# Kernel optimization log

Measured on AMD Instinct MI355X. Metric: run time of the kernel, lower is better.

Reference implementation:

```python
import jax, jax.numpy as jnp
import numpy as np

B_, S, D_IN, D_OUT, R = 4, 2048, 2048, 2048, 16

def setup_inputs() -> dict:
    key = jax.random.key(0)
    k = jax.random.split(key, 5)
    x = jax.random.normal(k[0], (B_, S, D_IN), dtype=jnp.float32)
    W = jax.random.normal(k[1], (D_OUT, D_IN), dtype=jnp.float32) * (1.0 / np.sqrt(D_IN))
    b = jax.random.normal(k[2], (D_OUT,), dtype=jnp.float32) * 0.02
    A = jax.random.normal(k[3], (R, D_IN), dtype=jnp.float32) * 0.02  # nn.init.normal_(std=0.02)
    Bm = jax.random.normal(k[4], (D_OUT, R), dtype=jnp.float32) * 0.02
    scale = jnp.asarray(0.8, dtype=jnp.float32)
    return {"x": x, "W": W, "b": b, "A": A, "B": Bm, "scale": scale}

def reference(x, W, b, A, B, scale):
    # base linear: y = x @ W^T + b
    orig = jnp.einsum('bsd,od->bso', x, W) + b
    # LoRA: scale * (x @ A^T) @ B^T
    h = jnp.einsum('bsd,rd->bsr', x, A)          # [B,S,r]
    lora = jnp.einsum('bsr,or->bso', h, B) * scale
    return orig + lora
```

## Files before the change

kernel.cpp:

```cpp
#include <hip/hip_runtime.h>
#include <hip/hip_bf16.h>
#include <cstdint>


typedef __bf16 bf16x8 __attribute__((ext_vector_type(8)));
typedef float floatx4 __attribute__((ext_vector_type(4)));
typedef unsigned short ushort8 __attribute__((ext_vector_type(8)));

#define BM 256
#define BN 256
#define BK 64
#define NT 32

__device__ __forceinline__ void gload_lds16(const void* g, void* l) {
    __builtin_amdgcn_global_load_lds((__attribute__((address_space(1))) void*)g,
                                     (__attribute__((address_space(3))) void*)l,
                                     16, 0, 0);
}

__device__ __forceinline__ unsigned short f2bf_bits(float f) {
    unsigned int u = __float_as_uint(f);
    u += 0x7FFFu + ((u >> 16) & 1u);
    return (unsigned short)(u >> 16);
}

__global__ __launch_bounds__(256)
void aux_kernel(const float* __restrict__ x, unsigned short* __restrict__ Xbf,
                const float* __restrict__ W, const float* __restrict__ A,
                const float* __restrict__ Bm, const float* __restrict__ scale_p,
                unsigned short* __restrict__ Weff)
{
    const int K = 2048, R = 16;
    int bid = blockIdx.x;
    if (bid < 8192) {
        size_t i = ((size_t)bid * 256 + threadIdx.x) * 8;
        float4 a = *reinterpret_cast<const float4*>(x + i);
        float4 b = *reinterpret_cast<const float4*>(x + i + 4);
        ushort8 o;
        o[0] = f2bf_bits(a.x); o[1] = f2bf_bits(a.y);
        o[2] = f2bf_bits(a.z); o[3] = f2bf_bits(a.w);
        o[4] = f2bf_bits(b.x); o[5] = f2bf_bits(b.y);
        o[6] = f2bf_bits(b.z); o[7] = f2bf_bits(b.w);
        *reinterpret_cast<ushort8*>(Xbf + i) = o;
    } else {
        int t  = (bid - 8192) * 256 + threadIdx.x;
        int n  = t >> 8;
        int k8 = (t & 255) << 3;

        float s = *scale_p;
        float br[16];
#pragma unroll
        for (int r = 0; r < R; ++r)
            br[r] = s * Bm[n * R + r];

        float acc[8] = {0,0,0,0,0,0,0,0};
#pragma unroll
        for (int r = 0; r < R; ++r) {
            const float* ap = A + r * K + k8;
#pragma unroll
            for (int j = 0; j < 8; ++j)
                acc[j] += br[r] * ap[j];
        }

        const float* wp = W + (size_t)n * K + k8;
        ushort8 o;
#pragma unroll
        for (int j = 0; j < 8; ++j)
            o[j] = f2bf_bits(wp[j] + acc[j]);
        *reinterpret_cast<ushort8*>(Weff + (size_t)n * K + k8) = o;
    }
}

#define BAR()       __builtin_amdgcn_s_barrier()
#define WAIT_LGKM() asm volatile("s_waitcnt lgkmcnt(0)" ::: "memory")
#define WAIT_VM4()  asm volatile("s_waitcnt vmcnt(4)" ::: "memory")
#define WAIT_VM0()  asm volatile("s_waitcnt vmcnt(0)" ::: "memory")

#define STAGE_A(buf, mh, kt) do {                                             \
    gload_lds16(gA0 + (size_t)(mh) * 64 * K + (kt) * 64, &Sa[buf][mh][c0 * 8]); \
    gload_lds16(gA1 + (size_t)(mh) * 64 * K + (kt) * 64, &Sa[buf][mh][c1 * 8]); \
} while (0)

#define STAGE_B(buf, nh, kt) do {                                             \
    gload_lds16(gB0 + (size_t)(nh) * 32 * K + (kt) * 64, &Sb[buf][nh][c0 * 8]); \
    gload_lds16(gB1 + (size_t)(nh) * 32 * K + (kt) * 64, &Sb[buf][nh][c1 * 8]); \
} while (0)

#define READ_A(buf, mh) do {                                                  \
    const unsigned short* ra = &Sa[buf][mh][(wr * 64 + lrow) * 64];           \
    _Pragma("unroll")                                                         \
    for (int mq = 0; mq < 4; ++mq) {                                          \
        af[0][mq] = *reinterpret_cast<const bf16x8*>(ra + mq * 1024 + swz0);  \
        af[1][mq] = *reinterpret_cast<const bf16x8*>(ra + mq * 1024 + swz1);  \
    }                                                                         \
} while (0)

#define READ_B(buf, nh) do {                                                  \
    const unsigned short* rb = &Sb[buf][nh][(wc * 32 + lrow) * 64];           \
    _Pragma("unroll")                                                         \
    for (int nq = 0; nq < 2; ++nq) {                                          \
        bq[0][nq] = *reinterpret_cast<const bf16x8*>(rb + nq * 1024 + swz0);  \
        bq[1][nq] = *reinterpret_cast<const bf16x8*>(rb + nq * 1024 + swz1);  \
    }                                                                         \
} while (0)

#define MFMAQ(mh, nh) do {                                                    \
    __builtin_amdgcn_s_setprio(1);                                            \
    _Pragma("unroll")                                                         \
    for (int mq = 0; mq < 4; ++mq)                                            \
        _Pragma("unroll")                                                     \
        for (int nq = 0; nq < 2; ++nq) {                                      \
            floatx4 tmp = __builtin_amdgcn_mfma_f32_16x16x32_bf16(            \
                af[0][mq], bq[0][nq], acc[(mh)*4+mq][(nh)*2+nq], 0, 0, 0);    \
            acc[(mh)*4+mq][(nh)*2+nq] = __builtin_amdgcn_mfma_f32_16x16x32_bf16( \
                af[1][mq], bq[1][nq], tmp, 0, 0, 0);                          \
        }                                                                     \
    __builtin_amdgcn_s_setprio(0);                                            \
} while (0)

__global__ __launch_bounds__(512)
void gemm_bias_kernel(const unsigned short* __restrict__ X,
                      const unsigned short* __restrict__ Wt,
                      const float* __restrict__ bias,
                      float* __restrict__ out)
{
    const int N = 2048, K = 2048;

    __shared__ alignas(16) unsigned short Sa[2][2][8192];
    __shared__ alignas(16) unsigned short Sb[2][2][8192];

    const int tid  = threadIdx.x;
    const int wave = tid >> 6;
    const int lane = tid & 63;
    const int lrow = lane & 15;
    const int quad = lane >> 4;
    const int wr   = wave >> 2;
    const int wc   = wave & 3;

    const int id  = blockIdx.x;
    const int xcd = id & 7;
    const int sg  = id >> 3;
    const int bm  = (xcd * 4 + (sg & 3)) * BM;
    const int bn  = (sg >> 2) * BN;

    const int c0 = tid, c1 = tid + 512;
    const int ar0 = (c0 >> 3) & 63, as0 = c0 & 7;
    const int ar1 = (c1 >> 3) & 63, as1 = c1 & 7;
    const unsigned short* gA0 = X + (size_t)(bm + (c0 >> 9) * 128 + ar0) * K
                                  + ((as0 ^ (ar0 & 7)) << 3);
    const unsigned short* gA1 = X + (size_t)(bm + (c1 >> 9) * 128 + ar1) * K
                                  + ((as1 ^ (ar1 & 7)) << 3);
    const int br0 = (c0 >> 3) & 31, br1 = (c1 >> 3) & 31;
    const unsigned short* gB0 = Wt + (size_t)(bn + (c0 >> 8) * 64 + br0) * K
                                   + ((as0 ^ (br0 & 7)) << 3);
    const unsigned short* gB1 = Wt + (size_t)(bn + (c1 >> 8) * 64 + br1) * K
                                   + ((as1 ^ (br1 & 7)) << 3);

    const int swz0 = (quad ^ (lrow & 7)) << 3;
    const int swz1 = swz0 ^ 32;

    floatx4 acc[8][4] = {};
    bf16x8 af[2][4];
    bf16x8 bq[2][2];

    STAGE_A(0, 0, 0);
    STAGE_B(0, 1, 0);
    STAGE_B(0, 0, 0);
    STAGE_A(0, 1, 0);
    STAGE_A(1, 0, 1);
    STAGE_B(1, 1, 1);
    WAIT_VM4(); BAR();

#pragma unroll 1
    for (int tt = 0; tt < NT; tt += 2) {
        const int t1 = tt + 1;
        const int t2 = (tt + 2 < NT) ? tt + 2 : NT - 1;
        const int t3 = (tt + 3 < NT) ? tt + 3 : NT - 1;

        READ_A(0, 0); READ_B(0, 0);
        STAGE_B(1, 0, t1);
        BAR(); WAIT_LGKM(); MFMAQ(0, 0); BAR();
        READ_B(0, 1);
        STAGE_A(1, 1, t1);
        BAR(); WAIT_LGKM(); MFMAQ(0, 1); BAR();
        READ_A(0, 1);
        STAGE_A(0, 0, t2);
        BAR(); WAIT_LGKM(); MFMAQ(1, 1); BAR();
        READ_B(0, 0);
        STAGE_B(0, 1, t2);
        BAR(); WAIT_LGKM(); MFMAQ(1, 0); WAIT_VM4(); BAR();

        READ_A(1, 0); READ_B(1, 0);
        STAGE_B(0, 0, t2);
        BAR(); WAIT_LGKM(); MFMAQ(0, 0); BAR();
        READ_B(1, 1);
        STAGE_A(0, 1, t2);
        BAR(); WAIT_LGKM(); MFMAQ(0, 1); BAR();
        READ_A(1, 1);
        STAGE_A(1, 0, t3);
        BAR(); WAIT_LGKM(); MFMAQ(1, 1); BAR();
        READ_B(1, 0);
        STAGE_B(1, 1, t3);
        BAR(); WAIT_LGKM(); MFMAQ(1, 0); WAIT_VM4(); BAR();
    }
    WAIT_VM0();

    float bsv[4];
#pragma unroll
    for (int ni = 0; ni < 4; ++ni)
        bsv[ni] = bias[bn + wc * 64 + (ni >> 1) * 32 + (ni & 1) * 16 + lrow];

    const int rbase = quad << 2;
#pragma unroll
    for (int mi = 0; mi < 8; ++mi) {
#pragma unroll
        for (int r = 0; r < 4; ++r) {
            size_t rowoff = (size_t)(bm + wr * 128 + (mi >> 2) * 64
                                     + (mi & 3) * 16 + rbase + r) * N;
#pragma unroll
            for (int ni = 0; ni < 4; ++ni)
                out[rowoff + bn + wc * 64 + (ni >> 1) * 32 + (ni & 1) * 16 + lrow]
                    = acc[mi][ni][r] + bsv[ni];
        }
    }
}

extern "C" void kernel_launch(void* const* d_in, const int* in_sizes, int n_in,
                              void* d_out, int out_size, void* d_ws, size_t ws_size,
                              hipStream_t stream)
{
    const float* x  = (const float*)d_in[0];
    const float* W  = (const float*)d_in[1];
    const float* b  = (const float*)d_in[2];
    const float* A  = (const float*)d_in[3];
    const float* Bm = (const float*)d_in[4];
    const float* sc = (const float*)d_in[5];
    float* out = (float*)d_out;

    const size_t M = 8192, N = 2048, K = 2048;

    unsigned short* Xbf  = (unsigned short*)d_ws;
    unsigned short* Weff = (unsigned short*)d_ws + M * K;

    aux_kernel<<<dim3((M * K + N * K) / 8 / 256), dim3(256), 0, stream>>>(
        x, Xbf, W, A, Bm, sc, Weff);

    gemm_bias_kernel<<<dim3((M / BM) * (N / BN)), dim3(512), 0, stream>>>(
        Xbf, Weff, b, out);
}
```

Measured before the change: 207.5 us.

## Fuse x fp32-to-bf16 conversion into GEMM A-tile loading via registers

Removes the separate pass that converted x to bf16 in a workspace. The GEMM now loads fp32 x tiles into registers, converts them to bf16 and writes them to swizzled LDS, interleaved with the MFMA phases. It also sets launch_bounds to allow two blocks per CU. The aim is to skip the write and re-read of a 32MB bf16 copy of x, at the cost of reading fp32 x (twice the bytes) several times across N-tiles, plus more register pressure and VALU work inside the main loop. The vmcnt waits were also dropped, so correctness now relies on the register-data dependencies and barriers.

```diff
diff --git a/kernel.cpp b/kernel.cpp
--- a/kernel.cpp
+++ b/kernel.cpp
@@ -25,65 +25,65 @@
 }
 
 __global__ __launch_bounds__(256)
-void aux_kernel(const float* __restrict__ x, unsigned short* __restrict__ Xbf,
-                const float* __restrict__ W, const float* __restrict__ A,
+void aux_kernel(const float* __restrict__ W, const float* __restrict__ A,
                 const float* __restrict__ Bm, const float* __restrict__ scale_p,
                 unsigned short* __restrict__ Weff)
 {
     const int K = 2048, R = 16;
-    int bid = blockIdx.x;
-    if (bid < 8192) {
-        size_t i = ((size_t)bid * 256 + threadIdx.x) * 8;
-        float4 a = *reinterpret_cast<const float4*>(x + i);
-        float4 b = *reinterpret_cast<const float4*>(x + i + 4);
-        ushort8 o;
-        o[0] = f2bf_bits(a.x); o[1] = f2bf_bits(a.y);
-        o[2] = f2bf_bits(a.z); o[3] = f2bf_bits(a.w);
-        o[4] = f2bf_bits(b.x); o[5] = f2bf_bits(b.y);
-        o[6] = f2bf_bits(b.z); o[7] = f2bf_bits(b.w);
-        *reinterpret_cast<ushort8*>(Xbf + i) = o;
-    } else {
-        int t  = (bid - 8192) * 256 + threadIdx.x;
-        int n  = t >> 8;
-        int k8 = (t & 255) << 3;
-
-        float s = *scale_p;
-        float br[16];
-#pragma unroll
-        for (int r = 0; r < R; ++r)
-            br[r] = s * Bm[n * R + r];
-
-        float acc[8] = {0,0,0,0,0,0,0,0};
-#pragma unroll
-        for (int r = 0; r < R; ++r) {
-            const float* ap = A + r * K + k8;
-#pragma unroll
-            for (int j = 0; j < 8; ++j)
-                acc[j] += br[r] * ap[j];
-        }
-
-        const float* wp = W + (size_t)n * K + k8;
-        ushort8 o;
+    int t  = blockIdx.x * 256 + threadIdx.x;
+    int n  = t >> 8;
+    int k8 = (t & 255) << 3;
+
+    float s = *scale_p;
+    float br[16];
+#pragma unroll
+    for (int r = 0; r < R; ++r)
+        br[r] = s * Bm[n * R + r];
+
+    float acc[8] = {0,0,0,0,0,0,0,0};
+#pragma unroll
+    for (int r = 0; r < R; ++r) {
+        const float* ap = A + r * K + k8;
 #pragma unroll
         for (int j = 0; j < 8; ++j)
-            o[j] = f2bf_bits(wp[j] + acc[j]);
-        *reinterpret_cast<ushort8*>(Weff + (size_t)n * K + k8) = o;
+            acc[j] += br[r] * ap[j];
     }
+
+    const float* wp = W + (size_t)n * K + k8;
+    ushort8 o;
+#pragma unroll
+    for (int j = 0; j < 8; ++j)
+        o[j] = f2bf_bits(wp[j] + acc[j]);
+    *reinterpret_cast<ushort8*>(Weff + (size_t)n * K + k8) = o;
 }
 
 #define BAR()       __builtin_amdgcn_s_barrier()
 #define WAIT_LGKM() asm volatile("s_waitcnt lgkmcnt(0)" ::: "memory")
-#define WAIT_VM4()  asm volatile("s_waitcnt vmcnt(4)" ::: "memory")
 #define WAIT_VM0()  asm volatile("s_waitcnt vmcnt(0)" ::: "memory")
 
-#define STAGE_A(buf, mh, kt) do {                                             \
-    gload_lds16(gA0 + (size_t)(mh) * 64 * K + (kt) * 64, &Sa[buf][mh][c0 * 8]); \
-    gload_lds16(gA1 + (size_t)(mh) * 64 * K + (kt) * 64, &Sa[buf][mh][c1 * 8]); \
-} while (0)
-
 #define STAGE_B(buf, nh, kt) do {                                             \
-    gload_lds16(gB0 + (size_t)(nh) * 32 * K + (kt) * 64, &Sb[buf][nh][c0 * 8]); \
-    gload_lds16(gB1 + (size_t)(nh) * 32 * K + (kt) * 64, &Sb[buf][nh][c1 * 8]); \
+    gload_lds16(gB0 + (size_t)(nh) * 32 * 2048 + (kt) * 64, &Sb[buf][nh][c0 * 8]); \
+    gload_lds16(gB1 + (size_t)(nh) * 32 * 2048 + (kt) * 64, &Sb[buf][nh][c1 * 8]); \
+} while (0)
+
+#define AISSUE(mh, kt) do {                                                   \
+    const float* xp = xA + (size_t)(mh) * 64 * 2048 + (kt) * 64;              \
+    q0 = *reinterpret_cast<const float4*>(xp);                                \
+    q1 = *reinterpret_cast<const float4*>(xp + 4);                            \
+    q2 = *reinterpret_cast<const float4*>(xp + 128 * 2048);                   \
+    q3 = *reinterpret_cast<const float4*>(xp + 128 * 2048 + 4);               \
+} while (0)
+
+#define AWRITE(buf, mh) do {                                                  \
+    ushort8 o0, o1;                                                           \
+    o0[0]=f2bf_bits(q0.x); o0[1]=f2bf_bits(q0.y); o0[2]=f2bf_bits(q0.z);      \
+    o0[3]=f2bf_bits(q0.w); o0[4]=f2bf_bits(q1.x); o0[5]=f2bf_bits(q1.y);      \
+    o0[6]=f2bf_bits(q1.z); o0[7]=f2bf_bits(q1.w);                             \
+    o1[0]=f2bf_bits(q2.x); o1[1]=f2bf_bits(q2.y); o1[2]=f2bf_bits(q2.z);      \
+    o1[3]=f2bf_bits(q2.w); o1[4]=f2bf_bits(q3.x); o1[5]=f2bf_bits(q3.y);      \
+    o1[6]=f2bf_bits(q3.z); o1[7]=f2bf_bits(q3.w);                             \
+    *reinterpret_cast<ushort8*>(&Sa[buf][mh][dstA])        = o0;              \
+    *reinterpret_cast<ushort8*>(&Sa[buf][mh][dstA + 4096]) = o1;              \
 } while (0)
 
 #define READ_A(buf, mh) do {                                                  \
@@ -118,8 +118,8 @@
     __builtin_amdgcn_s_setprio(0);                                            \
 } while (0)
 
-__global__ __launch_bounds__(512)
-void gemm_bias_kernel(const unsigned short* __restrict__ X,
+__global__ __launch_bounds__(512, 2)
+void gemm_bias_kernel(const float* __restrict__ x,
                       const unsigned short* __restrict__ Wt,
                       const float* __restrict__ bias,
                       float* __restrict__ out)
@@ -143,18 +143,18 @@
     const int bm  = (xcd * 4 + (sg & 3)) * BM;
     const int bn  = (sg >> 2) * BN;
 
+    const int ar = (tid >> 3) & 63;
+    const int as = tid & 7;
+    const float* xA = x + (size_t)(bm + ar) * K + as * 8;
+    const int dstA = ar * 64 + ((as ^ (ar & 7)) << 3);
+    float4 q0, q1, q2, q3;
+
     const int c0 = tid, c1 = tid + 512;
-    const int ar0 = (c0 >> 3) & 63, as0 = c0 & 7;
-    const int ar1 = (c1 >> 3) & 63, as1 = c1 & 7;
-    const unsigned short* gA0 = X + (size_t)(bm + (c0 >> 9) * 128 + ar0) * K
-                                  + ((as0 ^ (ar0 & 7)) << 3);
-    const unsigned short* gA1 = X + (size_t)(bm + (c1 >> 9) * 128 + ar1) * K
-                                  + ((as1 ^ (ar1 & 7)) << 3);
     const int br0 = (c0 >> 3) & 31, br1 = (c1 >> 3) & 31;
     const unsigned short* gB0 = Wt + (size_t)(bn + (c0 >> 8) * 64 + br0) * K
-                                   + ((as0 ^ (br0 & 7)) << 3);
+                                   + ((as ^ (br0 & 7)) << 3);
     const unsigned short* gB1 = Wt + (size_t)(bn + (c1 >> 8) * 64 + br1) * K
-                                   + ((as1 ^ (br1 & 7)) << 3);
+                                   + (((c1 & 7) ^ (br1 & 7)) << 3);
 
     const int swz0 = (quad ^ (lrow & 7)) << 3;
     const int swz1 = swz0 ^ 32;
@@ -163,13 +163,13 @@
     bf16x8 af[2][4];
     bf16x8 bq[2][2];
 
-    STAGE_A(0, 0, 0);
+    STAGE_B(0, 0, 0);
     STAGE_B(0, 1, 0);
-    STAGE_B(0, 0, 0);
-    STAGE_A(0, 1, 0);
-    STAGE_A(1, 0, 1);
     STAGE_B(1, 1, 1);
-    WAIT_VM4(); BAR();
+    AISSUE(0, 0); AWRITE(0, 0);
+    AISSUE(1, 0); AWRITE(0, 1);
+    AISSUE(0, 1); AWRITE(1, 0);
+    WAIT_VM0(); WAIT_LGKM(); BAR();
 
 #pragma unroll 1
     for (int tt = 0; tt < NT; tt += 2) {
@@ -179,29 +179,33 @@
 
         READ_A(0, 0); READ_B(0, 0);
         STAGE_B(1, 0, t1);
+        AISSUE(1, t1);
         BAR(); WAIT_LGKM(); MFMAQ(0, 0); BAR();
+        AWRITE(1, 1);
         READ_B(0, 1);
-        STAGE_A(1, 1, t1);
+        AISSUE(0, t2);
         BAR(); WAIT_LGKM(); MFMAQ(0, 1); BAR();
+        AWRITE(0, 0);
         READ_A(0, 1);
-        STAGE_A(0, 0, t2);
         BAR(); WAIT_LGKM(); MFMAQ(1, 1); BAR();
         READ_B(0, 0);
         STAGE_B(0, 1, t2);
-        BAR(); WAIT_LGKM(); MFMAQ(1, 0); WAIT_VM4(); BAR();
+        BAR(); WAIT_LGKM(); MFMAQ(1, 0); BAR();
 
         READ_A(1, 0); READ_B(1, 0);
         STAGE_B(0, 0, t2);
+        AISSUE(1, t2);
         BAR(); WAIT_LGKM(); MFMAQ(0, 0); BAR();
+        AWRITE(0, 1);
         READ_B(1, 1);
-        STAGE_A(0, 1, t2);
+        AISSUE(0, t3);
         BAR(); WAIT_LGKM(); MFMAQ(0, 1); BAR();
+        AWRITE(1, 0);
         READ_A(1, 1);
-        STAGE_A(1, 0, t3);
         BAR(); WAIT_LGKM(); MFMAQ(1, 1); BAR();
         READ_B(1, 0);
         STAGE_B(1, 1, t3);
-        BAR(); WAIT_LGKM(); MFMAQ(1, 0); WAIT_VM4(); BAR();
+        BAR(); WAIT_LGKM(); MFMAQ(1, 0); BAR();
     }
     WAIT_VM0();
 
@@ -239,12 +243,11 @@
 
     const size_t M = 8192, N = 2048, K = 2048;
 
-    unsigned short* Xbf  = (unsigned short*)d_ws;
-    unsigned short* Weff = (unsigned short*)d_ws + M * K;
-
-    aux_kernel<<<dim3((M * K + N * K) / 8 / 256), dim3(256), 0, stream>>>(
-        x, Xbf, W, A, Bm, sc, Weff);
+    unsigned short* Weff = (unsigned short*)d_ws;
+
+    aux_kernel<<<dim3(N * K / 8 / 256), dim3(256), 0, stream>>>(
+        W, A, Bm, sc, Weff);
 
     gemm_bias_kernel<<<dim3((M / BM) * (N / BN)), dim3(512), 0, stream>>>(
-        Xbf, Weff, b, out);
-}
+        x, Weff, b, out);
+}
```

Result: slower. 237.8 us (+14.6%).

## Switch GEMM inner loop to 32x32x16 MFMA tiles and drop redundant B reload

Applied to the files above, without the earlier changes.

Replaces the 16x16x32 bf16 MFMA with the 32x32x16 variant, giving each wave 4x2 tiles of 32x32 accumulators. The LDS read pattern and swizzle offsets are rewritten to match the new operand layout, and the epilogue is rewritten for the 32x32 output layout. B fragments are now held in two register sets, so the fourth READ_B in each half-iteration is removed. The aim is fewer MFMA issues and fewer LDS reads per K-step, at the cost of more live registers and a different, possibly less coalesced, store pattern.

```diff
diff --git a/kernel.cpp b/kernel.cpp
--- a/kernel.cpp
+++ b/kernel.cpp
@@ -4,7 +4,7 @@
 
 
 typedef __bf16 bf16x8 __attribute__((ext_vector_type(8)));
-typedef float floatx4 __attribute__((ext_vector_type(4)));
+typedef float floatx16 __attribute__((ext_vector_type(16)));
 typedef unsigned short ushort8 __attribute__((ext_vector_type(8)));
 
 #define BM 256
@@ -77,44 +77,40 @@
 #define WAIT_VM0()  asm volatile("s_waitcnt vmcnt(0)" ::: "memory")
 
 #define STAGE_A(buf, mh, kt) do {                                             \
-    gload_lds16(gA0 + (size_t)(mh) * 64 * K + (kt) * 64, &Sa[buf][mh][c0 * 8]); \
-    gload_lds16(gA1 + (size_t)(mh) * 64 * K + (kt) * 64, &Sa[buf][mh][c1 * 8]); \
+    gload_lds16(gA0 + (size_t)(mh) * 64 * 2048 + (kt) * 64, &Sa[buf][mh][c0 * 8]); \
+    gload_lds16(gA1 + (size_t)(mh) * 64 * 2048 + (kt) * 64, &Sa[buf][mh][c1 * 8]); \
 } while (0)
 
 #define STAGE_B(buf, nh, kt) do {                                             \
-    gload_lds16(gB0 + (size_t)(nh) * 32 * K + (kt) * 64, &Sb[buf][nh][c0 * 8]); \
-    gload_lds16(gB1 + (size_t)(nh) * 32 * K + (kt) * 64, &Sb[buf][nh][c1 * 8]); \
+    gload_lds16(gB0 + (size_t)(nh) * 32 * 2048 + (kt) * 64, &Sb[buf][nh][c0 * 8]); \
+    gload_lds16(gB1 + (size_t)(nh) * 32 * 2048 + (kt) * 64, &Sb[buf][nh][c1 * 8]); \
 } while (0)
 
 #define READ_A(buf, mh) do {                                                  \
-    const unsigned short* ra = &Sa[buf][mh][(wr * 64 + lrow) * 64];           \
+    const unsigned short* ra = &Sa[buf][mh][(wr * 64 + l31) * 64];            \
     _Pragma("unroll")                                                         \
-    for (int mq = 0; mq < 4; ++mq) {                                          \
-        af[0][mq] = *reinterpret_cast<const bf16x8*>(ra + mq * 1024 + swz0);  \
-        af[1][mq] = *reinterpret_cast<const bf16x8*>(ra + mq * 1024 + swz1);  \
+    for (int ks = 0; ks < 4; ++ks) {                                          \
+        af[0][ks] = *reinterpret_cast<const bf16x8*>(ra + swzk[ks]);          \
+        af[1][ks] = *reinterpret_cast<const bf16x8*>(ra + 2048 + swzk[ks]);   \
     }                                                                         \
 } while (0)
 
-#define READ_B(buf, nh) do {                                                  \
-    const unsigned short* rb = &Sb[buf][nh][(wc * 32 + lrow) * 64];           \
+#define READ_B(buf, nh, BQ) do {                                              \
+    const unsigned short* rb = &Sb[buf][nh][(wc * 32 + l31) * 64];            \
     _Pragma("unroll")                                                         \
-    for (int nq = 0; nq < 2; ++nq) {                                          \
-        bq[0][nq] = *reinterpret_cast<const bf16x8*>(rb + nq * 1024 + swz0);  \
-        bq[1][nq] = *reinterpret_cast<const bf16x8*>(rb + nq * 1024 + swz1);  \
-    }                                                                         \
-} while (0)
-
-#define MFMAQ(mh, nh) do {                                                    \
+    for (int ks = 0; ks < 4; ++ks)                                            \
+        BQ[ks] = *reinterpret_cast<const bf16x8*>(rb + swzk[ks]);             \
+} while (0)
+
+#define MFMAQ(mh, nh, BQ) do {                                                \
     __builtin_amdgcn_s_setprio(1);                                            \
     _Pragma("unroll")                                                         \
-    for (int mq = 0; mq < 4; ++mq)                                            \
-        _Pragma("unroll")                                                     \
-        for (int nq = 0; nq < 2; ++nq) {                                      \
-            floatx4 tmp = __builtin_amdgcn_mfma_f32_16x16x32_bf16(            \
-                af[0][mq], bq[0][nq], acc[(mh)*4+mq][(nh)*2+nq], 0, 0, 0);    \
-            acc[(mh)*4+mq][(nh)*2+nq] = __builtin_amdgcn_mfma_f32_16x16x32_bf16( \
-                af[1][mq], bq[1][nq], tmp, 0, 0, 0);                          \
-        }                                                                     \
+    for (int ks = 0; ks < 4; ++ks) {                                          \
+        acc[(mh)*2+0][nh] = __builtin_amdgcn_mfma_f32_32x32x16_bf16(          \
+            af[0][ks], BQ[ks], acc[(mh)*2+0][nh], 0, 0, 0);                   \
+        acc[(mh)*2+1][nh] = __builtin_amdgcn_mfma_f32_32x32x16_bf16(          \
+            af[1][ks], BQ[ks], acc[(mh)*2+1][nh], 0, 0, 0);                   \
+    }                                                                         \
     __builtin_amdgcn_s_setprio(0);                                            \
 } while (0)
 
@@ -132,8 +128,9 @@
     const int tid  = threadIdx.x;
     const int wave = tid >> 6;
     const int lane = tid & 63;
-    const int lrow = lane & 15;
-    const int quad = lane >> 4;
+    const int l31  = lane & 31;
+    const int kg   = lane >> 5;
+    const int l7   = lane & 7;
     const int wr   = wave >> 2;
     const int wc   = wave & 3;
 
@@ -156,12 +153,12 @@
     const unsigned short* gB1 = Wt + (size_t)(bn + (c1 >> 8) * 64 + br1) * K
                                    + ((as1 ^ (br1 & 7)) << 3);
 
-    const int swz0 = (quad ^ (lrow & 7)) << 3;
-    const int swz1 = swz0 ^ 32;
-
-    floatx4 acc[8][4] = {};
+    const int swzk[4] = { ((0 + kg) ^ l7) << 3, ((2 + kg) ^ l7) << 3,
+                          ((4 + kg) ^ l7) << 3, ((6 + kg) ^ l7) << 3 };
+
+    floatx16 acc[4][2] = {};
     bf16x8 af[2][4];
-    bf16x8 bq[2][2];
+    bf16x8 bqa[4], bqb[4];
 
     STAGE_A(0, 0, 0);
     STAGE_B(0, 1, 0);
@@ -177,50 +174,43 @@
         const int t2 = (tt + 2 < NT) ? tt + 2 : NT - 1;
         const int t3 = (tt + 3 < NT) ? tt + 3 : NT - 1;
 
-        READ_A(0, 0); READ_B(0, 0);
+        READ_A(0, 0); READ_B(0, 0, bqa);
         STAGE_B(1, 0, t1);
-        BAR(); WAIT_LGKM(); MFMAQ(0, 0); BAR();
-        READ_B(0, 1);
+        BAR(); WAIT_LGKM(); MFMAQ(0, 0, bqa); BAR();
+        READ_B(0, 1, bqb);
         STAGE_A(1, 1, t1);
-        BAR(); WAIT_LGKM(); MFMAQ(0, 1); BAR();
+        BAR(); WAIT_LGKM(); MFMAQ(0, 1, bqb); BAR();
         READ_A(0, 1);
         STAGE_A(0, 0, t2);
-        BAR(); WAIT_LGKM(); MFMAQ(1, 1); BAR();
-        READ_B(0, 0);
+        BAR(); WAIT_LGKM(); MFMAQ(1, 1, bqb); BAR();
         STAGE_B(0, 1, t2);
-        BAR(); WAIT_LGKM(); MFMAQ(1, 0); WAIT_VM4(); BAR();
-
-        READ_A(1, 0); READ_B(1, 0);
+        BAR(); WAIT_LGKM(); MFMAQ(1, 0, bqa); WAIT_VM4(); BAR();
+
+        READ_A(1, 0); READ_B(1, 0, bqa);
         STAGE_B(0, 0, t2);
-        BAR(); WAIT_LGKM(); MFMAQ(0, 0); BAR();
-        READ_B(1, 1);
+        BAR(); WAIT_LGKM(); MFMAQ(0, 0, bqa); BAR();
+        READ_B(1, 1, bqb);
         STAGE_A(0, 1, t2);
-        BAR(); WAIT_LGKM(); MFMAQ(0, 1); BAR();
+        BAR(); WAIT_LGKM(); MFMAQ(0, 1, bqb); BAR();
         READ_A(1, 1);
         STAGE_A(1, 0, t3);
-        BAR(); WAIT_LGKM(); MFMAQ(1, 1); BAR();
-        READ_B(1, 0);
+        BAR(); WAIT_LGKM(); MFMAQ(1, 1, bqb); BAR();
         STAGE_B(1, 1, t3);
-        BAR(); WAIT_LGKM(); MFMAQ(1, 0); WAIT_VM4(); BAR();
+        BAR(); WAIT_LGKM(); MFMAQ(1, 0, bqa); WAIT_VM4(); BAR();
     }
     WAIT_VM0();
 
-    float bsv[4];
-#pragma unroll
-    for (int ni = 0; ni < 4; ++ni)
-        bsv[ni] = bias[bn + wc * 64 + (ni >> 1) * 32 + (ni & 1) * 16 + lrow];
-
-    const int rbase = quad << 2;
-#pragma unroll
-    for (int mi = 0; mi < 8; ++mi) {
-#pragma unroll
-        for (int r = 0; r < 4; ++r) {
-            size_t rowoff = (size_t)(bm + wr * 128 + (mi >> 2) * 64
-                                     + (mi & 3) * 16 + rbase + r) * N;
-#pragma unroll
-            for (int ni = 0; ni < 4; ++ni)
-                out[rowoff + bn + wc * 64 + (ni >> 1) * 32 + (ni & 1) * 16 + lrow]
-                    = acc[mi][ni][r] + bsv[ni];
+    const float bsv0 = bias[bn + wc * 64 + l31];
+    const float bsv1 = bias[bn + wc * 64 + 32 + l31];
+    const size_t cb  = (size_t)bn + wc * 64 + l31;
+#pragma unroll
+    for (int mb = 0; mb < 4; ++mb) {
+#pragma unroll
+        for (int r = 0; r < 16; ++r) {
+            size_t rowoff = (size_t)(bm + wr * 128 + mb * 32
+                                     + (r & 3) + ((r >> 2) << 3) + (kg << 2)) * N;
+            out[rowoff + cb]      = acc[mb][0][r] + bsv0;
+            out[rowoff + cb + 32] = acc[mb][1][r] + bsv1;
         }
     }
 }
```

Result: no change. 210.4 us (+1.4%).
